# Performance work log

Measured on AMD Instinct MI355X. Metric: run time of the kernel, lower is better.

The kernel has to match this reference:

```python
import jax, jax.numpy as jnp
import numpy as np

K = 1024        # num_embeddings
D = 256         # embedding_dim
B, T = 64, 512  # batch, time -> N = 32768 flattened vectors
S = 5           # num_samples
DECAY = 0.999
EPS = 1e-5
COMMIT = 0.25


def setup_inputs() -> dict:
    key = jax.random.key(0)
    k1, k2 = jax.random.split(key)
    x = jax.random.normal(k1, (B, T, D), dtype=jnp.float32)
    # nn.init.uniform_(weight, -1/512, 1/512)
    embedding = jax.random.uniform(k2, (K, D), dtype=jnp.float32, minval=-1.0 / 512, maxval=1.0 / 512)
    ema_count = jnp.zeros((K,), dtype=jnp.float32)
    ema_weight = embedding  # buffer initialized as a clone of the weight
    return {"x": x, "embedding": embedding, "ema_count": ema_count, "ema_weight": ema_weight}


def reference(x, embedding, ema_count, ema_weight):
    N = x.shape[0] * x.shape[1]
    xf = x.reshape(-1, D)                      # [N, D]
    xf_sg = jax.lax.stop_gradient(xf)
    w = jax.lax.stop_gradient(embedding)       # [K, D]

    distances = (jnp.sum(w * w, axis=1)[None, :]
                 + jnp.sum(xf_sg * xf_sg, axis=1, keepdims=True)
                 - 2.0 * (xf_sg @ w.T))

    # categorical sampling with logits = -distances, S samples per row -> [S, N]
    skey = jax.random.key(42)
    samples = jax.random.categorical(skey, -distances, axis=-1, shape=(S, N))

    # mean of S one-hots without materializing [S, N, K] one-hot tensor
    encodings = jnp.zeros((N, K), dtype=jnp.float32).at[jnp.arange(N)[None, :], samples].add(1.0 / S)

    # EMA codebook update (training path; all under no_grad in torch)
    new_count = DECAY * ema_count + (1.0 - DECAY) * jnp.sum(encodings, axis=0)
    n = jnp.sum(new_count)
    new_count = (new_count + EPS) / (n + K * EPS) * n
    dw = encodings.T @ xf_sg                   # [K, D]
    new_weight = DECAY * ema_weight + (1.0 - DECAY) * dw
    new_embedding = new_weight / new_count[:, None]

    # gather with the UPDATED codebook, mean over samples -> [N, D]
    quantized = jnp.mean(new_embedding[samples], axis=0).reshape(x.shape)
    quantized = jax.lax.stop_gradient(quantized)

    e_latent_loss = jnp.mean((x - quantized) ** 2)
    loss = COMMIT * e_latent_loss

    quantized_st = x + jax.lax.stop_gradient(quantized - x)  # straight-through

    avg_probs = jnp.mean(encodings, axis=0)
    perplexity = jnp.exp(-jnp.sum(avg_probs * jnp.log(avg_probs + 1e-10)))

    return quantized_st, loss, perplexity, new_embedding, new_count, new_weight
```

## Files before the change

kernel.cpp:

```cpp
#include <hip/hip_runtime.h>
#include <stdint.h>
#include <math.h>

#define NV 32768
#define DIM 256
#define KCB 1024
#define NSAMP 5

typedef double f64x4 __attribute__((ext_vector_type(4)));
typedef float  f32x4v __attribute__((ext_vector_type(4)));
typedef short  bf16x8 __attribute__((ext_vector_type(8)));

__device__ __forceinline__ uint32_t rotl32(uint32_t v, int r) {
  return (v << r) | (v >> (32 - r));
}

__device__ __forceinline__ void threefry2x32(uint32_t c0, uint32_t c1,
                                             uint32_t& o0, uint32_t& o1) {
  const uint32_t k0 = 0u, k1 = 42u;
  const uint32_t k2 = k0 ^ k1 ^ 0x1BD11BDAu;
  uint32_t x0 = c0 + k0, x1 = c1 + k1;
  x0 += x1; x1 = rotl32(x1, 13); x1 ^= x0;
  x0 += x1; x1 = rotl32(x1, 15); x1 ^= x0;
  x0 += x1; x1 = rotl32(x1, 26); x1 ^= x0;
  x0 += x1; x1 = rotl32(x1,  6); x1 ^= x0;
  x0 += k1; x1 += k2 + 1u;
  x0 += x1; x1 = rotl32(x1, 17); x1 ^= x0;
  x0 += x1; x1 = rotl32(x1, 29); x1 ^= x0;
  x0 += x1; x1 = rotl32(x1, 16); x1 ^= x0;
  x0 += x1; x1 = rotl32(x1, 24); x1 ^= x0;
  x0 += k2; x1 += k0 + 2u;
  x0 += x1; x1 = rotl32(x1, 13); x1 ^= x0;
  x0 += x1; x1 = rotl32(x1, 15); x1 ^= x0;
  x0 += x1; x1 = rotl32(x1, 26); x1 ^= x0;
  x0 += x1; x1 = rotl32(x1,  6); x1 ^= x0;
  x0 += k0; x1 += k1 + 3u;
  x0 += x1; x1 = rotl32(x1, 17); x1 ^= x0;
  x0 += x1; x1 = rotl32(x1, 29); x1 ^= x0;
  x0 += x1; x1 = rotl32(x1, 16); x1 ^= x0;
  x0 += x1; x1 = rotl32(x1, 24); x1 ^= x0;
  x0 += k1; x1 += k2 + 4u;
  x0 += x1; x1 = rotl32(x1, 13); x1 ^= x0;
  x0 += x1; x1 = rotl32(x1, 15); x1 ^= x0;
  x0 += x1; x1 = rotl32(x1, 26); x1 ^= x0;
  x0 += x1; x1 = rotl32(x1,  6); x1 ^= x0;
  x0 += k2; x1 += k0 + 5u;
  o0 = x0; o1 = x1;
}

__device__ __forceinline__ float neg_log_f32(float xf) {
  uint32_t i = __float_as_uint(xf);
  int e = ((int)(i - 0x3f3504f3u)) >> 23;
  double m = (double)__uint_as_float(i - (uint32_t)(e << 23));
  double z = (m - 1.0) / (m + 1.0);
  double p = z * z;
  double poly = 0x1.1111111111111p-4;
  poly = fma(poly, p, 0x1.3b13b13b13b14p-4);
  poly = fma(poly, p, 0x1.745d1745d1746p-4);
  poly = fma(poly, p, 0x1.c71c71c71c71cp-4);
  poly = fma(poly, p, 0x1.2492492492492p-3);
  poly = fma(poly, p, 0x1.999999999999ap-3);
  poly = fma(poly, p, 0x1.5555555555555p-2);
  poly = fma(poly, p, 1.0);
  double r = fma(-2.0 * z, poly, (double)(-e) * 0x1.62e42fefa39efp-1);
  return (float)r;
}

__device__ __forceinline__ float u_from_bits(uint32_t bits) {
  uint32_t m = bits >> 9;
  return (m == 0u) ? 1.17549435e-38f
                   : (__uint_as_float(m | 0x3f800000u) - 1.0f);
}

__device__ __forceinline__ float gumbel_exact(uint32_t bits) {
  float u = u_from_bits(bits);
  float t = neg_log_f32(u);
  return neg_log_f32(t);
}

__device__ __forceinline__ float gumbel_approx(uint32_t bits) {
  float u = u_from_bits(bits);
  float t = __log2f(u) * (-0.6931471805599453f);
  return __log2f(t) * (-0.6931471805599453f);
}

#define E2G 4e-5f

__device__ __forceinline__ uint32_t f2bf(float f) {
  uint32_t b = __float_as_uint(f);
  return (b + 0x7fffu + ((b >> 16) & 1u)) >> 16;
}
__device__ __forceinline__ float bf2f(uint32_t h) {
  return __uint_as_float(h << 16);
}


__global__ __launch_bounds__(256) void k_decomp(const float* __restrict__ src,
                                                ushort* __restrict__ b0,
                                                ushort* __restrict__ b1,
                                                ushort* __restrict__ b2,
                                                float* __restrict__ sums) {
  __shared__ float xl[16 * 260];
  int r0 = blockIdx.x * 16;
  int t = threadIdx.x;
#pragma unroll
  for (int i = 0; i < 16; ++i) {
    float v = src[(size_t)(r0 + i) * 256 + t];
    xl[i * 260 + t] = v;
    uint32_t h0 = f2bf(v);
    float f0 = bf2f(h0);
    float r1 = v - f0;
    uint32_t h1 = f2bf(r1);
    float f1 = bf2f(h1);
    float r2 = r1 - f1;
    uint32_t h2 = f2bf(r2);
    size_t o = (size_t)(r0 + i) * 256 + t;
    b0[o] = (ushort)h0; b1[o] = (ushort)h1; b2[o] = (ushort)h2;
  }
  __syncthreads();
  if (t < 16) {
    const float* p = xl + t * 260;
    float acc = 0.0f;
    for (int i = 0; i < 256; ++i)
      acc = __fadd_rn(acc, __fmul_rn(p[i], p[i]));
    sums[r0 + t] = acc;
  }
}

__global__ __launch_bounds__(256) void k_prep64(const float* __restrict__ emb,
                                                double* __restrict__ wT64) {
  __shared__ float tile[64][65];
  int bk = blockIdx.x;
  int bd = blockIdx.y;
  int t = threadIdx.x;
  int tr = t >> 6, tc = t & 63;
#pragma unroll
  for (int i = 0; i < 16; ++i) {
    int kk = tr + i * 4;
    tile[kk][tc] = emb[(size_t)(bk * 64 + kk) * 256 + bd * 64 + tc];
  }
  __syncthreads();
#pragma unroll
  for (int i = 0; i < 16; ++i) {
    int dd = tr + i * 4;
    wT64[(size_t)(bd * 64 + dd) * 1024 + bk * 64 + tc] = (double)tile[tc][dd];
  }
}

__global__ __launch_bounds__(256) void k_rowsumsq(const float* __restrict__ a,
                                                  float* __restrict__ outp,
                                                  int rows) {
  int r = blockIdx.x * blockDim.x + threadIdx.x;
  if (r >= rows) return;
  const float* p = a + (size_t)r * DIM;
  float acc = 0.0f;
  for (int i = 0; i < DIM; ++i) {
    float pi = p[i];
    acc = __fadd_rn(acc, __fmul_rn(pi, pi));
  }
  outp[r] = acc;
}


__global__ __launch_bounds__(256) void k_logits_bf(
    const ushort* __restrict__ xb0, const ushort* __restrict__ xb1,
    const ushort* __restrict__ xb2,
    const ushort* __restrict__ wp0, const ushort* __restrict__ wp1,
    const ushort* __restrict__ wp2,
    const float* __restrict__ wsum, const float* __restrict__ xsum,
    float* __restrict__ logits, int chunkbase) {
  int t = threadIdx.x;
  int l = t & 63, wid = t >> 6;
  int rows0 = blockIdx.x * 64 + wid * 16;
  int lrow = l & 15, lk = l >> 4;

  bf16x8 a0[8], a1[8], a2[8];
  {
    size_t rb = (size_t)(rows0 + lrow) * 256 + (size_t)lk * 8;
#pragma unroll
    for (int ch = 0; ch < 8; ++ch) {
      a0[ch] = *reinterpret_cast<const bf16x8*>(xb0 + rb + ch * 32);
      a1[ch] = *reinterpret_cast<const bf16x8*>(xb1 + rb + ch * 32);
      a2[ch] = *reinterpret_cast<const bf16x8*>(xb2 + rb + ch * 32);
    }
  }
  float xs4[4];
#pragma unroll
  for (int r = 0; r < 4; ++r)
    xs4[r] = xsum[chunkbase + rows0 + lk * 4 + r];

#pragma unroll 1
  for (int strip = 0; strip < 16; ++strip) {
    int col0 = strip * 64;
    f32x4v acc0 = {0.f, 0.f, 0.f, 0.f};
    f32x4v acc1 = {0.f, 0.f, 0.f, 0.f};
    f32x4v acc2 = {0.f, 0.f, 0.f, 0.f};
    f32x4v acc3 = {0.f, 0.f, 0.f, 0.f};

#define KT_STEP(ACC, KT)                                                      \
    {                                                                         \
      size_t wb = (size_t)(col0 + (KT) * 16 + lrow) * 256 + ch * 32 + lk * 8; \
      bf16x8 fb0 = *reinterpret_cast<const bf16x8*>(wp0 + wb);                \
      bf16x8 fb1 = *reinterpret_cast<const bf16x8*>(wp1 + wb);                \
      bf16x8 fb2 = *reinterpret_cast<const bf16x8*>(wp2 + wb);                \
      ACC = __builtin_amdgcn_mfma_f32_16x16x32_bf16(a0[ch], fb0, ACC, 0,0,0); \
      ACC = __builtin_amdgcn_mfma_f32_16x16x32_bf16(a0[ch], fb1, ACC, 0,0,0); \
      ACC = __builtin_amdgcn_mfma_f32_16x16x32_bf16(a1[ch], fb0, ACC, 0,0,0); \
      ACC = __builtin_amdgcn_mfma_f32_16x16x32_bf16(a1[ch], fb1, ACC, 0,0,0); \
      ACC = __builtin_amdgcn_mfma_f32_16x16x32_bf16(a0[ch], fb2, ACC, 0,0,0); \
      ACC = __builtin_amdgcn_mfma_f32_16x16x32_bf16(a2[ch], fb0, ACC, 0,0,0); \
    }

#pragma unroll
    for (int ch = 0; ch < 8; ++ch) {
      KT_STEP(acc0, 0)
      KT_STEP(acc1, 1)
      KT_STEP(acc2, 2)
      KT_STEP(acc3, 3)
    }
#undef KT_STEP

#pragma unroll
    for (int kt = 0; kt < 4; ++kt) {
      f32x4v acc = (kt == 0) ? acc0 : (kt == 1) ? acc1 : (kt == 2) ? acc2 : acc3;
      int col = col0 + kt * 16 + lrow;
      float ws_k = wsum[col];
#pragma unroll
      for (int r = 0; r < 4; ++r) {
        int row = rows0 + lk * 4 + r;
        float l32 = __fsub_rn(__fmul_rn(2.0f, acc[r]),
                              __fadd_rn(ws_k, xs4[r]));
        logits[(size_t)row * 1024 + col] = l32;
      }
    }
  }
}

__global__ __launch_bounds__(256) void k_sampler(const float* __restrict__ logits,
                                                 int* __restrict__ samples,
                                                 int* __restrict__ cnt,
                                                 int chunkbase) {
  int t = threadIdx.x;
  int p = t & 15;
  int rloc = blockIdx.x * 16 + (t >> 4);
  int row = chunkbase + rloc;
  uint32_t rowk = (uint32_t)row * 1024u;

  const float4* lp = (const float4*)(logits + (size_t)rloc * 1024) + p;

  float    wvt[NSAMP];
  int      wk[NSAMP], rk[NSAMP];
  uint32_t wbits[NSAMP], rbits[NSAMP];
  uint32_t rmask = 0;
#pragma unroll
  for (int s = 0; s < NSAMP; ++s) {
    wvt[s] = -INFINITY; wk[s] = 0; wbits[s] = 0u; rk[s] = 0; rbits[s] = 0u;
  }

#pragma unroll 1
  for (int j = 0; j < 16; ++j) {
    float4 f = lp[(size_t)j * 16];
    float lvs[4] = {f.x, f.y, f.z, f.w};
    int kb = 4 * p + 64 * j;
#pragma unroll
    for (int e = 0; e < 4; ++e) {
      int k = kb + e;
      float lv = lvs[e];
      uint32_t cbase = rowk + (uint32_t)k;
#pragma unroll
      for (int s = 0; s < NSAMP; ++s) {
        uint32_t o0, o1;
        threefry2x32(0u, cbase + (uint32_t)s * 33554432u, o0, o1);
        uint32_t bits = o0 ^ o1;
        float u = __uint_as_float((bits >> 9) | 0x3f800000u) - 1.0f;
        float tt = __log2f(u) * (-0.6931471805599453f);
        float g  = __log2f(tt) * (-0.6931471805599453f);
        float vt = __fadd_rn(g, lv);
        float wpre = wvt[s];
        float d = vt - wpre;
        if (fabsf(d) < E2G) {
          bool up = vt > wpre;
          rk[s]    = up ? wk[s]    : k;
          rbits[s] = up ? wbits[s] : bits;
          rmask |= (1u << s);
        }
        bool gt = vt > wpre;
        wvt[s]   = gt ? vt   : wpre;
        wk[s]    = gt ? k    : wk[s];
        wbits[s] = gt ? bits : wbits[s];
      }
    }
  }

  const float* lrow_p = logits + (size_t)rloc * 1024;
#pragma unroll
  for (int s = 0; s < NSAMP; ++s) {
    float ev = __fadd_rn(gumbel_exact(wbits[s]), lrow_p[wk[s]]);
    int ek = wk[s];
    if (rmask & (1u << s)) {
      float er = __fadd_rn(gumbel_exact(rbits[s]), lrow_p[rk[s]]);
      if (er > ev || (er == ev && rk[s] < ek)) { ev = er; ek = rk[s]; }
    }
#pragma unroll
    for (int off = 1; off < 16; off <<= 1) {
      float v2 = __shfl_xor(ev, off, 64);
      int   k2 = __shfl_xor(ek, off, 64);
      if (v2 > ev || (v2 == ev && k2 < ek)) { ev = v2; ek = k2; }
    }
    if (p == 0) {
      samples[s * NV + row] = ek;
      atomicAdd(&cnt[ek], 1);
    }
  }
}

__global__ __launch_bounds__(256) void k_fused(const float* __restrict__ x,
                                               const double* __restrict__ wT64,
                                               const float* __restrict__ wsum,
                                               const float* __restrict__ xsum,
                                               int* __restrict__ samples,
                                               int* __restrict__ cnt) {
  __shared__ float xl[16 * 260];
  __shared__ float ll[256 * 17];
  __shared__ float xs[16];
  __shared__ float vred[4 * 16 * 5];
  __shared__ int   kred[4 * 16 * 5];

  int nb = blockIdx.x;
  int t = threadIdx.x;
  int lane = t & 63, wv = t >> 6;
  int m = lane & 15, g = lane >> 4;
  int r = t & 15, kg = t >> 4;

#pragma unroll
  for (int i = 0; i < 16; ++i)
    xl[i * 260 + t] = x[((size_t)nb * 16 + i) * 256 + t];
  if (t < 16) xs[t] = xsum[nb * 16 + t];
  __syncthreads();

  float    wvt[NSAMP], wlv[NSAMP], rlv[NSAMP];
  int      wk[NSAMP], rk[NSAMP];
  uint32_t wbits[NSAMP], rbits[NSAMP];
  uint32_t rvmask = 0;
#pragma unroll
  for (int s = 0; s < NSAMP; ++s) {
    wvt[s] = -INFINITY; wlv[s] = 0.f; wk[s] = 0; wbits[s] = 0u;
    rlv[s] = 0.f; rk[s] = 0; rbits[s] = 0u;
  }
  uint32_t rowbase = ((uint32_t)nb * 16u + (uint32_t)r) * 1024u;

  for (int ch = 0; ch < 4; ++ch) {
    for (int ct = 0; ct < 4; ++ct) {
      int klocal = wv * 64 + ct * 16 + m;
      int kglob = ch * 256 + klocal;
      f64x4 C = {0.0, 0.0, 0.0, 0.0};
      const double* bp = wT64 + (size_t)g * 1024 + kglob;
      const float* ap = xl + m * 260 + g;
#pragma unroll 8
      for (int step = 0; step < 64; ++step) {
        double a = (double)ap[step * 4];
        double b = bp[(size_t)step * 4096];
        C = __builtin_amdgcn_mfma_f64_16x16x4f64(a, b, C, 0, 0, 0);
      }
      float ws_k = wsum[kglob];
#pragma unroll
      for (int j = 0; j < 4; ++j) {
        int row = g * 4 + j;
        float l32 = __fsub_rn(__fmul_rn(2.0f, (float)C[j]),
                              __fadd_rn(ws_k, xs[row]));
        ll[klocal * 17 + row] = l32;
      }
    }
    __syncthreads();
#pragma unroll 1
    for (int i = 0; i < 16; ++i) {
      int kl = kg + (i << 4);
      float lv = ll[kl * 17 + r];
      int gki = (ch << 8) + kl;
      uint32_t cbase = rowbase + (uint32_t)gki;
#pragma unroll
      for (int s = 0; s < NSAMP; ++s) {
        uint32_t o0, o1;
        threefry2x32(0u, cbase + (uint32_t)s * 33554432u, o0, o1);
        uint32_t bits = o0 ^ o1;
        float vt = __fadd_rn(gumbel_approx(bits), lv);
        if (vt > wvt[s]) {
          if (wvt[s] > vt - E2G) {
            rk[s] = wk[s]; rbits[s] = wbits[s]; rlv[s] = wlv[s];
            rvmask |= (1u << s);
          }
          wvt[s] = vt; wk[s] = gki; wbits[s] = bits; wlv[s] = lv;
        } else if (vt > wvt[s] - E2G) {
          rk[s] = gki; rbits[s] = bits; rlv[s] = lv;
          rvmask |= (1u << s);
        }
      }
    }
    __syncthreads();
  }

#pragma unroll
  for (int s = 0; s < NSAMP; ++s) {
    float ev = __fadd_rn(gumbel_exact(wbits[s]), wlv[s]);
    int ek = wk[s];
    if (rvmask & (1u << s)) {
      float er = __fadd_rn(gumbel_exact(rbits[s]), rlv[s]);
      if (er > ev || (er == ev && rk[s] < ek)) { ev = er; ek = rk[s]; }
    }
#pragma unroll
    for (int off = 16; off <= 32; off <<= 1) {
      float v2 = __shfl_xor(ev, off, 64);
      int   k2 = __shfl_xor(ek, off, 64);
      if (v2 > ev || (v2 == ev && k2 < ek)) { ev = v2; ek = k2; }
    }
    if (g == 0) {
      vred[(wv * 16 + r) * 5 + s] = ev;
      kred[(wv * 16 + r) * 5 + s] = ek;
    }
  }
  __syncthreads();
  if (t < 80) {
    int rr = t / 5, s = t % 5;
    float best = vred[rr * 5 + s];
    int bk2 = kred[rr * 5 + s];
#pragma unroll
    for (int w = 1; w < 4; ++w) {
      float v2 = vred[(w * 16 + rr) * 5 + s];
      int   k2 = kred[(w * 16 + rr) * 5 + s];
      if (v2 > best || (v2 == best && k2 < bk2)) { best = v2; bk2 = k2; }
    }
    int n = nb * 16 + rr;
    samples[s * NV + n] = bk2;
    atomicAdd(&cnt[bk2], 1);
  }
}


__global__ __launch_bounds__(1024) void k_meta(const float* __restrict__ ema_count,
                                               const int* __restrict__ cnt,
                                               int* __restrict__ offs,
                                               int* __restrict__ cursor,
                                               double* __restrict__ ncn64,
                                               float* __restrict__ out_count,
                                               float* __restrict__ out_perp) {
  __shared__ int sc[1024];
  __shared__ double red[1024];
  int k = threadIdx.x;
  int v = cnt[k];
  sc[k] = v;
  __syncthreads();
  for (int off = 1; off < 1024; off <<= 1) {
    int a = (k >= off) ? sc[k - off] : 0;
    __syncthreads();
    sc[k] += a;
    __syncthreads();
  }
  int excl = sc[k] - v;
  offs[k] = excl;
  cursor[k] = excl;

  double ec = (double)v * 0.2;
  double nc0 = 0.999 * (double)ema_count[k] + 0.001 * ec;
  red[k] = nc0;
  __syncthreads();
  for (int off = 512; off > 0; off >>= 1) {
    if (k < off) red[k] += red[k + off];
    __syncthreads();
  }
  double ntot = red[0];
  __syncthreads();
  double ncn = (nc0 + 1e-5) / (ntot + (double)KCB * 1e-5) * ntot;
  ncn64[k] = ncn;
  out_count[k] = (float)ncn;

  double avg = ec / (double)NV;
  red[k] = avg * log(avg + 1e-10);
  __syncthreads();
  for (int off = 512; off > 0; off >>= 1) {
    if (k < off) red[k] += red[k + off];
    __syncthreads();
  }
  if (k == 0) out_perp[0] = (float)exp(-red[0]);
}

__global__ __launch_bounds__(256) void k_fill(const int* __restrict__ samples,
                                              int* __restrict__ cursor,
                                              uint32_t* __restrict__ list) {
  int idx = blockIdx.x * 256 + threadIdx.x;
  int k = samples[idx];
  int n = idx & (NV - 1);
  int pos = atomicAdd(&cursor[k], 1);
  list[pos] = (uint32_t)n;
}

__global__ __launch_bounds__(256) void k_weight2(const float* __restrict__ x,
                                                 const float* __restrict__ ema_w,
                                                 const uint32_t* __restrict__ list,
                                                 const int* __restrict__ offs,
                                                 const int* __restrict__ cnt,
                                                 const double* __restrict__ ncn64,
                                                 float* __restrict__ out_w,
                                                 float* __restrict__ out_emb,
                                                 float* __restrict__ emb32) {
  int k = blockIdx.x, d = threadIdx.x;
  const uint32_t* lp = list + offs[k];
  int mcnt = cnt[k];
  double acc0 = 0.0, acc1 = 0.0;
  int i = 0;
  for (; i + 2 <= mcnt; i += 2) {
    uint32_t n0 = lp[i], n1 = lp[i + 1];
    acc0 += (double)x[(size_t)n0 * 256 + d];
    acc1 += (double)x[(size_t)n1 * 256 + d];
  }
  if (i < mcnt) acc0 += (double)x[(size_t)lp[i] * 256 + d];
  double dw = 0.2 * (acc0 + acc1);
  double nw = 0.999 * (double)ema_w[(size_t)k * 256 + d] + 0.001 * dw;
  float nw32 = (float)nw;
  float e = __fdiv_rn(nw32, (float)ncn64[k]);
  size_t i2 = (size_t)k * 256 + d;
  out_w[i2] = nw32;
  out_emb[i2] = e;
  emb32[i2] = e;
}

__global__ __launch_bounds__(256) void k_quant(const float* __restrict__ x,
                                               const int* __restrict__ samples,
                                               const float* __restrict__ emb32,
                                               float* __restrict__ out_q,
                                               double* __restrict__ lossacc) {
  __shared__ int s5[16][5];
  __shared__ double wred[4];
  int bid = blockIdx.x;
  int t = threadIdx.x;
  if (t < 80) {
    int rr = t / 5, s = t % 5;
    s5[rr][s] = samples[s * NV + bid * 16 + rr];
  }
  __syncthreads();
  double lacc = 0.0;
#pragma unroll 1
  for (int rr = 0; rr < 16; ++rr) {
    size_t n = (size_t)bid * 16 + rr;
    float xv = x[n * DIM + t];
    float acc = emb32[(size_t)s5[rr][0] * DIM + t];
#pragma unroll
    for (int s = 1; s < NSAMP; ++s)
      acc = __fadd_rn(acc, emb32[(size_t)s5[rr][s] * DIM + t]);
    float q = __fdiv_rn(acc, 5.0f);
    out_q[n * DIM + t] = __fadd_rn(xv, __fsub_rn(q, xv));
    float df = __fsub_rn(xv, q);
    lacc += (double)df * (double)df;
  }
  for (int off = 32; off > 0; off >>= 1) lacc += __shfl_down(lacc, off, 64);
  int wid = t >> 6, lane = t & 63;
  if (lane == 0) wred[wid] = lacc;
  __syncthreads();
  if (t == 0) {
    double b = wred[0] + wred[1] + wred[2] + wred[3];
    __hip_atomic_fetch_add(lossacc, b, __ATOMIC_RELAXED, __HIP_MEMORY_SCOPE_AGENT);
  }
}

__global__ void k_loss(const double* __restrict__ lossacc,
                       float* __restrict__ out_loss) {
  out_loss[0] = (float)(0.25 * (lossacc[0] / (double)(NV * DIM)));
}

extern "C" void kernel_launch(void* const* d_in, const int* in_sizes, int n_in,
                              void* d_out, int out_size, void* d_ws, size_t ws_size,
                              hipStream_t stream) {
  const float* x     = (const float*)d_in[0];
  const float* emb   = (const float*)d_in[1];
  const float* ema_c = (const float*)d_in[2];
  const float* ema_w = (const float*)d_in[3];

  float* out      = (float*)d_out;
  float* out_q    = out;
  float* out_loss = out + 8388608;
  float* out_perp = out + 8388609;
  float* out_emb  = out + 8388610;
  float* out_cnt  = out + 8650754;
  float* out_w    = out + 8651778;

  char* ws = (char*)d_ws;

  ushort*   wb0     = (ushort*)(ws + 0);
  ushort*   wb1     = (ushort*)(ws + 524288);
  ushort*   wb2     = (ushort*)(ws + 1048576);
  float*    wsum    = (float*)(ws + 1572864);
  float*    xsum    = (float*)(ws + 1576960);
  int*      samples = (int*)(ws + 1708032);
  int*      cnt     = (int*)(ws + 2363392);
  double*   lossacc = (double*)(ws + 2367488);
  double*   ncn64   = (double*)(ws + 2367496);
  int*      offs    = (int*)(ws + 2375688);
  int*      cursor  = (int*)(ws + 2379784);
  uint32_t* list    = (uint32_t*)(ws + 2383880);
  float*    emb32   = (float*)(ws + 3039240);
  const size_t CB   = 4088064;

  size_t avail = (ws_size > CB) ? (ws_size - CB) : 0;
  size_t maxr = (avail / 5632) & ~(size_t)63;
  int chunk_rows = (maxr > (size_t)NV) ? NV : (int)maxr;
  bool split = (chunk_rows >= 8192);

  if (split) {
    ushort* xb0 = (ushort*)(ws + CB);
    ushort* xb1 = xb0 + (size_t)chunk_rows * 256;
    ushort* xb2 = xb1 + (size_t)chunk_rows * 256;
    float*  logits = (float*)(ws + CB + (size_t)chunk_rows * 1536);

    hipMemsetAsync(ws + 2363392, 0, 4104, stream);
    k_decomp<<<KCB / 16, 256, 0, stream>>>(emb, wb0, wb1, wb2, wsum);
    for (int base = 0; base < NV; base += chunk_rows) {
      int rows = (NV - base < chunk_rows) ? (NV - base) : chunk_rows;
      k_decomp<<<rows / 16, 256, 0, stream>>>(x + (size_t)base * 256,
                                              xb0, xb1, xb2, xsum + base);
      k_logits_bf<<<rows / 64, 256, 0, stream>>>(xb0, xb1, xb2,
                                                 wb0, wb1, wb2,
                                                 wsum, xsum, logits, base);
      k_sampler<<<rows / 16, 256, 0, stream>>>(logits, samples, cnt, base);
    }
    k_meta<<<1, 1024, 0, stream>>>(ema_c, cnt, offs, cursor, ncn64,
                                   out_cnt, out_perp);
    k_fill<<<NV * NSAMP / 256, 256, 0, stream>>>(samples, cursor, list);
    k_weight2<<<KCB, 256, 0, stream>>>(x, ema_w, list, offs, cnt, ncn64,
                                       out_w, out_emb, emb32);
    k_quant<<<NV / 16, 256, 0, stream>>>(x, samples, emb32, out_q, lossacc);
    k_loss<<<1, 1, 0, stream>>>(lossacc, out_loss);
  } else {
    double*   wT64_f    = (double*)(ws + 0);
    float*    wsum_f    = (float*)(ws + 2097152);
    float*    xsum_f    = (float*)(ws + 2101248);
    int*      samples_f = (int*)(ws + 2232320);
    int*      cnt_f     = (int*)(ws + 2887680);
    double*   lossacc_f = (double*)(ws + 2891776);
    double*   ncn64_f   = (double*)(ws + 2891784);
    int*      offs_f    = (int*)(ws + 2899976);
    int*      cursor_f  = (int*)(ws + 2904072);
    uint32_t* list_f    = (uint32_t*)(ws + 2908168);
    float*    emb32_f   = (float*)(ws + 3563528);

    hipMemsetAsync(ws + 2887680, 0, 4096 + 8, stream);
    k_prep64<<<dim3(16, 4), 256, 0, stream>>>(emb, wT64_f);
    k_rowsumsq<<<KCB / 256, 256, 0, stream>>>(emb, wsum_f, KCB);
    k_rowsumsq<<<NV / 256, 256, 0, stream>>>(x, xsum_f, NV);
    k_fused<<<NV / 16, 256, 0, stream>>>(x, wT64_f, wsum_f, xsum_f,
                                         samples_f, cnt_f);
    k_meta<<<1, 1024, 0, stream>>>(ema_c, cnt_f, offs_f, cursor_f, ncn64_f,
                                   out_cnt, out_perp);
    k_fill<<<NV * NSAMP / 256, 256, 0, stream>>>(samples_f, cursor_f, list_f);
    k_weight2<<<KCB, 256, 0, stream>>>(x, ema_w, list_f, offs_f, cnt_f, ncn64_f,
                                       out_w, out_emb, emb32_f);
    k_quant<<<NV / 16, 256, 0, stream>>>(x, samples_f, emb32_f, out_q, lossacc_f);
    k_loss<<<1, 1, 0, stream>>>(lossacc_f, out_loss);
  }
}
```

Measured before the change: 874.1 us.

## Split logits kernel columns across waves and reload x hi/lo parts per strip

Each block of the bf16 logits GEMM now covers 32 rows instead of 64. Two waves share a 16-row group and each handles half of the 1024 codebook columns, which doubles the grid. The second and third bf16 split parts of x are no longer held in registers for the whole kernel; they are reloaded every strip, and launch bounds now ask for 4 blocks per SM. The aim is to free registers to raise occupancy and parallelism, at the price of extra global or L2 loads of the x parts.

```diff
diff --git a/kernel.cpp b/kernel.cpp
--- a/kernel.cpp
+++ b/kernel.cpp
@@ -162,7 +162,7 @@
 }
 
 
-__global__ __launch_bounds__(256) void k_logits_bf(
+__global__ __launch_bounds__(256, 4) void k_logits_bf(
     const ushort* __restrict__ xb0, const ushort* __restrict__ xb1,
     const ushort* __restrict__ xb2,
     const ushort* __restrict__ wp0, const ushort* __restrict__ wp1,
@@ -171,54 +171,53 @@
     float* __restrict__ logits, int chunkbase) {
   int t = threadIdx.x;
   int l = t & 63, wid = t >> 6;
-  int rows0 = blockIdx.x * 64 + wid * 16;
+  int rg = wid >> 1, chf = wid & 1;
+  int rows0 = blockIdx.x * 32 + rg * 16;
   int lrow = l & 15, lk = l >> 4;
 
-  bf16x8 a0[8], a1[8], a2[8];
-  {
-    size_t rb = (size_t)(rows0 + lrow) * 256 + (size_t)lk * 8;
-#pragma unroll
-    for (int ch = 0; ch < 8; ++ch) {
-      a0[ch] = *reinterpret_cast<const bf16x8*>(xb0 + rb + ch * 32);
-      a1[ch] = *reinterpret_cast<const bf16x8*>(xb1 + rb + ch * 32);
-      a2[ch] = *reinterpret_cast<const bf16x8*>(xb2 + rb + ch * 32);
-    }
-  }
+  size_t rb = (size_t)(rows0 + lrow) * 256 + (size_t)lk * 8;
+  bf16x8 a0[8];
+#pragma unroll
+  for (int ch = 0; ch < 8; ++ch)
+    a0[ch] = *reinterpret_cast<const bf16x8*>(xb0 + rb + ch * 32);
+
   float xs4[4];
 #pragma unroll
   for (int r = 0; r < 4; ++r)
     xs4[r] = xsum[chunkbase + rows0 + lk * 4 + r];
 
 #pragma unroll 1
-  for (int strip = 0; strip < 16; ++strip) {
-    int col0 = strip * 64;
+  for (int strip = 0; strip < 8; ++strip) {
+    int col0 = chf * 512 + strip * 64;
     f32x4v acc0 = {0.f, 0.f, 0.f, 0.f};
     f32x4v acc1 = {0.f, 0.f, 0.f, 0.f};
     f32x4v acc2 = {0.f, 0.f, 0.f, 0.f};
     f32x4v acc3 = {0.f, 0.f, 0.f, 0.f};
 
+#pragma unroll
+    for (int ch = 0; ch < 8; ++ch) {
+      bf16x8 a1c = *reinterpret_cast<const bf16x8*>(xb1 + rb + ch * 32);
+      bf16x8 a2c = *reinterpret_cast<const bf16x8*>(xb2 + rb + ch * 32);
+
 #define KT_STEP(ACC, KT)                                                      \
-    {                                                                         \
-      size_t wb = (size_t)(col0 + (KT) * 16 + lrow) * 256 + ch * 32 + lk * 8; \
-      bf16x8 fb0 = *reinterpret_cast<const bf16x8*>(wp0 + wb);                \
-      bf16x8 fb1 = *reinterpret_cast<const bf16x8*>(wp1 + wb);                \
-      bf16x8 fb2 = *reinterpret_cast<const bf16x8*>(wp2 + wb);                \
-      ACC = __builtin_amdgcn_mfma_f32_16x16x32_bf16(a0[ch], fb0, ACC, 0,0,0); \
-      ACC = __builtin_amdgcn_mfma_f32_16x16x32_bf16(a0[ch], fb1, ACC, 0,0,0); \
-      ACC = __builtin_amdgcn_mfma_f32_16x16x32_bf16(a1[ch], fb0, ACC, 0,0,0); \
-      ACC = __builtin_amdgcn_mfma_f32_16x16x32_bf16(a1[ch], fb1, ACC, 0,0,0); \
-      ACC = __builtin_amdgcn_mfma_f32_16x16x32_bf16(a0[ch], fb2, ACC, 0,0,0); \
-      ACC = __builtin_amdgcn_mfma_f32_16x16x32_bf16(a2[ch], fb0, ACC, 0,0,0); \
-    }
-
-#pragma unroll
-    for (int ch = 0; ch < 8; ++ch) {
+      {                                                                       \
+        size_t wb = (size_t)(col0 + (KT)*16 + lrow) * 256 + ch * 32 + lk * 8; \
+        bf16x8 fb0 = *reinterpret_cast<const bf16x8*>(wp0 + wb);              \
+        bf16x8 fb1 = *reinterpret_cast<const bf16x8*>(wp1 + wb);              \
+        bf16x8 fb2 = *reinterpret_cast<const bf16x8*>(wp2 + wb);              \
+        ACC = __builtin_amdgcn_mfma_f32_16x16x32_bf16(a0[ch], fb0, ACC,0,0,0);\
+        ACC = __builtin_amdgcn_mfma_f32_16x16x32_bf16(a0[ch], fb1, ACC,0,0,0);\
+        ACC = __builtin_amdgcn_mfma_f32_16x16x32_bf16(a1c,    fb0, ACC,0,0,0);\
+        ACC = __builtin_amdgcn_mfma_f32_16x16x32_bf16(a1c,    fb1, ACC,0,0,0);\
+        ACC = __builtin_amdgcn_mfma_f32_16x16x32_bf16(a0[ch], fb2, ACC,0,0,0);\
+        ACC = __builtin_amdgcn_mfma_f32_16x16x32_bf16(a2c,    fb0, ACC,0,0,0);\
+      }
       KT_STEP(acc0, 0)
       KT_STEP(acc1, 1)
       KT_STEP(acc2, 2)
       KT_STEP(acc3, 3)
-    }
 #undef KT_STEP
+    }
 
 #pragma unroll
     for (int kt = 0; kt < 4; ++kt) {
@@ -616,7 +615,7 @@
       int rows = (NV - base < chunk_rows) ? (NV - base) : chunk_rows;
       k_decomp<<<rows / 16, 256, 0, stream>>>(x + (size_t)base * 256,
                                               xb0, xb1, xb2, xsum + base);
-      k_logits_bf<<<rows / 64, 256, 0, stream>>>(xb0, xb1, xb2,
+      k_logits_bf<<<rows / 32, 256, 0, stream>>>(xb0, xb1, xb2,
                                                  wb0, wb1, wb2,
                                                  wsum, xsum, logits, base);
       k_sampler<<<rows / 16, 256, 0, stream>>>(logits, samples, cnt, base);
```

New measurement: 1.026 ms. 17.4% more time.
